# Performance work log

Hardware: AMD Instinct MI355X
Metric: run time of the kernel (lower is better)

Reference implementation:

```python
import jax, jax.numpy as jnp
import numpy as np

DIM = 512
DEPTH = 6
HEADS = 8
DH = 64
WS = 256
INNER = HEADS * DH  # 512
FF_INNER = int(DIM * 4 * 2 / 3)  # 1365
QK_SCALE = 8.0


def l2norm(x):
    n = jnp.linalg.norm(x, axis=-1, keepdims=True)
    return x / jnp.maximum(n, 1e-12)


def rotate_half(x):
    x1, x2 = jnp.split(x, 2, axis=-1)
    return jnp.concatenate([-x2, x1], axis=-1)


def apply_xpos_rotary(q, k, n, dh, scale_base):
    # SinusoidalEmbeddings with use_xpos=True, scale_base = window_size // 2
    inv_freq = 1.0 / (10000.0 ** (jnp.arange(0, dh, 2, dtype=jnp.float32) / dh))  # (dh/2,)
    t = jnp.arange(n, dtype=jnp.float32)
    freqs = t[:, None] * inv_freq[None, :]                     # (n, dh/2)
    freqs = jnp.concatenate([freqs, freqs], axis=-1)           # (n, dh)
    sv = (jnp.arange(0, dh, 2, dtype=jnp.float32) + 0.4 * dh) / (1.4 * dh)  # (dh/2,)
    power = (t - n // 2) / scale_base
    xs = sv[None, :] ** power[:, None]                         # (n, dh/2)
    xs = jnp.concatenate([xs, xs], axis=-1)                    # (n, dh)
    cos, sin = jnp.cos(freqs), jnp.sin(freqs)
    q = q * cos * xs + rotate_half(q) * sin * xs
    k = k * cos / xs + rotate_half(k) * sin / xs
    return q, k


def local_mha(x, Wqkv, Wo, q_scale, k_scale):
    b, n, d = x.shape
    qkv = x @ Wqkv                                             # (b, n, 3*INNER)
    q, k, v = jnp.split(qkv, 3, axis=-1)
    to_heads = lambda t: t.reshape(b, n, HEADS, DH).transpose(0, 2, 1, 3)
    q, k, v = to_heads(q), to_heads(k), to_heads(v)            # (b, h, n, dh)
    # qk rmsnorm (l2 norm + learned per-dim scale), fixed attn scale = 8
    q = l2norm(q) * q_scale
    k = l2norm(k) * k_scale
    q, k = apply_xpos_rotary(q, k, n, DH, WS // 2)
    w = n // WS
    bucket = lambda t: t.reshape(b, HEADS, w, WS, DH)
    bq, bk, bv = bucket(q), bucket(k), bucket(v)
    # look_around: prepend previous window (look_backward=1, look_forward=0)
    def look_around(t):
        prev = jnp.concatenate([jnp.zeros_like(t[:, :, :1]), t[:, :, :-1]], axis=2)
        return jnp.concatenate([prev, t], axis=3)              # (b, h, w, 2*WS, dh)
    bk2, bv2 = look_around(bk), look_around(bv)
    # positions and masks (causal + exact windowsize + pad)
    tq = jnp.arange(n, dtype=jnp.int32).reshape(w, WS)
    tk_prev = jnp.concatenate([jnp.full((1, WS), -1, dtype=jnp.int32), tq[:-1]], axis=0)
    tk = jnp.concatenate([tk_prev, tq], axis=1)                # (w, 2*WS)
    diff = tq[:, :, None] - tk[:, None, :]
    allowed = (diff >= 0) & (diff <= WS) & (tk[:, None, :] >= 0)  # (w, WS, 2*WS)
    sim = jnp.einsum('bhwie,bhwje->bhwij', bq, bk2) * QK_SCALE
    sim = jnp.where(allowed, sim, -jnp.finfo(sim.dtype).max)
    attn = jax.nn.softmax(sim, axis=-1)
    o = jnp.einsum('bhwij,bhwje->bhwie', attn, bv2)            # (b, h, w, WS, dh)
    o = o.reshape(b, HEADS, n, DH).transpose(0, 2, 1, 3).reshape(b, n, INNER)
    return o @ Wo


def feedforward(x, W1, b1, W2, b2):
    h = x @ W1 + b1
    a, g = jnp.split(h, 2, axis=-1)
    return (a * jax.nn.gelu(g, approximate=False)) @ W2 + b2


def setup_inputs() -> dict:
    key = jax.random.key(0)
    ks = jax.random.split(key, 8)
    s = 0.02
    x = jax.random.normal(ks[0], (1, 8192, DIM), dtype=jnp.float32)
    Wqkv = jax.random.normal(ks[1], (DEPTH, DIM, 3 * INNER), dtype=jnp.float32) * s
    Wo = jax.random.normal(ks[2], (DEPTH, INNER, DIM), dtype=jnp.float32) * s
    q_scale = jnp.ones((DEPTH, DH), dtype=jnp.float32)
    k_scale = jnp.ones((DEPTH, DH), dtype=jnp.float32)
    W1 = jax.random.normal(ks[3], (DEPTH, DIM, 2 * FF_INNER), dtype=jnp.float32) * s
    b1 = jnp.zeros((DEPTH, 2 * FF_INNER), dtype=jnp.float32)
    W2 = jax.random.normal(ks[4], (DEPTH, FF_INNER, DIM), dtype=jnp.float32) * s
    b2 = jnp.zeros((DEPTH, DIM), dtype=jnp.float32)
    return {"x": x, "Wqkv": Wqkv, "Wo": Wo, "q_scale": q_scale, "k_scale": k_scale,
            "W1": W1, "b1": b1, "W2": W2, "b2": b2}


def reference(x, Wqkv, Wo, q_scale, k_scale, W1, b1, W2, b2):
    for i in range(DEPTH):
        x = local_mha(x, Wqkv[i], Wo[i], q_scale[i], k_scale[i]) + x
        x = feedforward(x, W1[i], b1[i], W2[i], b2[i]) + x
    return x
```

## Files before the change

### kernel.cpp

```cpp
#include <hip/hip_runtime.h>
#include <hip/hip_bf16.h>
#include <math.h>

typedef short s16x8 __attribute__((ext_vector_type(8)));
typedef short s16x4 __attribute__((ext_vector_type(4)));
typedef float f32x4 __attribute__((ext_vector_type(4)));

#define MFMA(A,B,C) __builtin_amdgcn_mfma_f32_16x16x32_bf16((A),(B),(C),0,0,0)

typedef __attribute__((address_space(3))) unsigned int lds_u32;
typedef __attribute__((address_space(1))) const unsigned int glb_u32;
__device__ __forceinline__ void gload16(const short* g, const short* l){
  __builtin_amdgcn_global_load_lds((glb_u32*)g, (lds_u32*)l, 16, 0, 0);
}

__device__ __forceinline__ float bf2f(short u){
  unsigned int x = ((unsigned int)(unsigned short)u) << 16;
  return __builtin_bit_cast(float, x);
}
__device__ __forceinline__ short f2bf(float f){
  unsigned int x = __builtin_bit_cast(unsigned int, f);
  x += 0x7fffu + ((x >> 16) & 1u);
  return (short)(x >> 16);
}
__device__ __forceinline__ float gelu_t(float x){
  float u = x + 0.044715f*x*x*x;
  float e = __expf(1.5957691216057308f*u);
  float th = 1.f - 2.f/(e + 1.f);
  return 0.5f*x*(1.f + th);
}

__device__ __forceinline__ void xcd_swz(int gx, int gy, int &bx, int &by){
  int id = bx + by*gx;
  int nwg = gx*gy;
  int q = nwg >> 3, r = nwg & 7;
  int xcd = id & 7, idx = id >> 3;
  int nid = (xcd < r ? xcd*(q+1) : r*(q+1) + (xcd-r)*q) + idx;
  bx = nid % gx; by = nid / gx;
}

#define FFI 1365
#define FFIP 1376

template<int HAS_BIAS, int HAS_RES, int OUT_F32, int OUT_BF16>
__global__ __launch_bounds__(512) void gemm_k(
    const short* __restrict__ A, const short* __restrict__ Bt,
    const float* __restrict__ bias, const float* __restrict__ res,
    float* __restrict__ outF, short* __restrict__ outB,
    int M, int N, int K)
{
  __shared__ short As[2][128*32];
  __shared__ short Bs[2][128*32];
  const int tid = threadIdx.x;
  const int lane = tid & 63, wv = tid >> 6;
  const int g = lane >> 4, qi = lane & 15;
  int bx = blockIdx.x, by = blockIdx.y;
  xcd_swz(gridDim.x, gridDim.y, bx, by);
  const int m0 = bx * 128, n0 = by * 128;
  const int wm = (wv >> 2) * 64, wn = (wv & 3) * 32;

  const int sr = tid >> 2, sc = (tid & 3) * 8;
  const short* Ag = A  + (size_t)(m0 + sr)*K + sc;
  const short* Bg = Bt + (size_t)(n0 + sr)*K + sc;

  f32x4 acc[4][2];
  #pragma unroll
  for (int i=0;i<4;i++)
    #pragma unroll
    for (int j=0;j<2;j++) acc[i][j] = (f32x4){0.f,0.f,0.f,0.f};

  auto stage = [&](int buf, int k0){
    gload16(Ag + k0, &As[buf][wv*512]);
    gload16(Bg + k0, &Bs[buf][wv*512]);
  };

  const int nt = K >> 5;
  stage(0, 0);
  __syncthreads();
  for (int t = 0; t < nt; ++t) {
    const int cur = t & 1;
    if (t + 1 < nt) stage(cur ^ 1, (t+1) << 5);
    s16x8 af[4], bf[2];
    #pragma unroll
    for (int mi=0;mi<4;mi++) af[mi] = *(const s16x8*)&As[cur][(wm+mi*16+qi)*32 + g*8];
    #pragma unroll
    for (int ni=0;ni<2;ni++) bf[ni] = *(const s16x8*)&Bs[cur][(wn+ni*16+qi)*32 + g*8];
    #pragma unroll
    for (int mi=0;mi<4;mi++)
      #pragma unroll
      for (int ni=0;ni<2;ni++)
        acc[mi][ni] = MFMA(af[mi], bf[ni], acc[mi][ni]);
    __syncthreads();
  }
  #pragma unroll
  for (int mi=0;mi<4;mi++){
    #pragma unroll
    for (int r=0;r<4;r++){
      int row = m0 + wm + mi*16 + g*4 + r;
      #pragma unroll
      for (int ni=0;ni<2;ni++){
        int col = n0 + wn + ni*16 + qi;
        float v = acc[mi][ni][r];
        if (HAS_BIAS) v += bias[col];
        if (HAS_RES)  v += res[(size_t)row*N + col];
        if (OUT_F32)  outF[(size_t)row*N + col] = v;
        if (OUT_BF16) outB[(size_t)row*N + col] = f2bf(v);
      }
    }
  }
}

__global__ __launch_bounds__(512) void geglu_k(
    const short* __restrict__ A, const short* __restrict__ Bt,
    const float* __restrict__ b1, short* __restrict__ hg)
{
  __shared__ short As[2][128*32];
  __shared__ short Ba[2][128*32];
  __shared__ short Bg[2][128*32];
  const int tid = threadIdx.x;
  const int lane = tid & 63, wv = tid >> 6;
  const int g = lane >> 4, qi = lane & 15;
  int bx = blockIdx.x, by = blockIdx.y;
  xcd_swz(gridDim.x, gridDim.y, bx, by);
  const int m0 = bx * 128, n0 = by * 128;
  const int wm = (wv >> 2) * 64, wn = (wv & 3) * 32;

  const int sr = tid >> 2, sc = (tid & 3) * 8;
  const short* Ag = A + (size_t)(m0 + sr)*512 + sc;
  const short* Pa = Bt + (size_t)min(n0 + sr, FFI-1)*512 + sc;
  const short* Pg = Bt + (size_t)min(FFI + n0 + sr, 2729)*512 + sc;

  f32x4 aa[4][2], ag[4][2];
  #pragma unroll
  for (int i=0;i<4;i++)
    #pragma unroll
    for (int j=0;j<2;j++){ aa[i][j]=(f32x4){0.f,0.f,0.f,0.f}; ag[i][j]=(f32x4){0.f,0.f,0.f,0.f}; }

  auto stage = [&](int buf, int k0){
    gload16(Ag + k0, &As[buf][wv*512]);
    gload16(Pa + k0, &Ba[buf][wv*512]);
    gload16(Pg + k0, &Bg[buf][wv*512]);
  };

  stage(0, 0);
  __syncthreads();
  for (int t = 0; t < 16; ++t) {
    const int cur = t & 1;
    if (t + 1 < 16) stage(cur ^ 1, (t+1) << 5);
    s16x8 af[4], bfa[2], bfg[2];
    #pragma unroll
    for (int mi=0;mi<4;mi++) af[mi] = *(const s16x8*)&As[cur][(wm+mi*16+qi)*32 + g*8];
    #pragma unroll
    for (int ni=0;ni<2;ni++){ bfa[ni] = *(const s16x8*)&Ba[cur][(wn+ni*16+qi)*32 + g*8];
                              bfg[ni] = *(const s16x8*)&Bg[cur][(wn+ni*16+qi)*32 + g*8]; }
    #pragma unroll
    for (int mi=0;mi<4;mi++)
      #pragma unroll
      for (int ni=0;ni<2;ni++){
        aa[mi][ni] = MFMA(af[mi], bfa[ni], aa[mi][ni]);
        ag[mi][ni] = MFMA(af[mi], bfg[ni], ag[mi][ni]);
      }
    __syncthreads();
  }
  #pragma unroll
  for (int mi=0;mi<4;mi++){
    #pragma unroll
    for (int r=0;r<4;r++){
      int row = m0 + wm + mi*16 + g*4 + r;
      #pragma unroll
      for (int ni=0;ni<2;ni++){
        int col = n0 + wn + ni*16 + qi;
        if (col < FFI){
          float va = aa[mi][ni][r] + b1[col];
          float vg = ag[mi][ni][r] + b1[FFI+col];
          hg[(size_t)row*FFIP + col] = f2bf(va * gelu_t(vg));
        } else if (col < FFIP){
          hg[(size_t)row*FFIP + col] = 0;
        }
      }
    }
  }
}

__global__ void rope_k(float* __restrict__ tab){
  int n = blockIdx.x, dd = threadIdx.x;
  int i = dd & 31;
  double invf = pow(10000.0, -(double)i/32.0);
  double fr = (double)n * invf;
  double c = cos(fr), s = sin(fr);
  double sv = (2.0*i + 25.6)/89.6;
  double pw = ((double)n - 4096.0)/128.0;
  double xs = pow(sv, pw);
  size_t o = (size_t)n*64 + dd;
  tab[o]            = (float)(c*xs);
  tab[524288+o]     = (float)(s*xs);
  tab[2*524288+o]   = (float)(c/xs);
  tab[3*524288+o]   = (float)(s/xs);
}

__global__ __launch_bounds__(256) void wtrans_k(
    const float* __restrict__ src, short* __restrict__ dst,
    int K, int N, int Kp, long srcStride, long dstStride)
{
  __shared__ float t[64][65];
  const float* s = src + (size_t)blockIdx.z * srcStride;
  short* d = dst + (size_t)blockIdx.z * dstStride;
  int n0 = blockIdx.x*64, k0 = blockIdx.y*64;
  int tid = threadIdx.x;
  #pragma unroll
  for (int p=0;p<4;p++){
    int task = p*256+tid;
    int r = task>>4, c = (task&15)*4;
    int k = k0 + r;
    #pragma unroll
    for (int e=0;e<4;e++){
      int n = n0+c+e;
      t[r][c+e] = (k<K && n<N) ? s[(size_t)k*N+n] : 0.f;
    }
  }
  __syncthreads();
  #pragma unroll
  for (int p=0;p<2;p++){
    int task = p*256+tid;
    int nr = task>>3, kg=(task&7)*8;
    int n = n0+nr;
    if (n < N && (k0+kg) < Kp){
      s16x8 v;
      #pragma unroll
      for (int j=0;j<8;j++) v[j] = f2bf(t[kg+j][nr]);
      *(s16x8*)(d + (size_t)n*Kp + k0 + kg) = v;
    }
  }
}

__global__ void cast_k(const float* __restrict__ in, short* __restrict__ out){
  int i = (blockIdx.x*256+threadIdx.x)*4;
  float4 v = *(const float4*)(in+i);
  s16x4 o = { f2bf(v.x), f2bf(v.y), f2bf(v.z), f2bf(v.w) };
  *(s16x4*)(out+i) = o;
}

__global__ __launch_bounds__(256) void qkprep_k(
    const short* __restrict__ qkv, const float* __restrict__ tab,
    const float* __restrict__ qs, const float* __restrict__ ks,
    short* __restrict__ qrot, short* __restrict__ krot)
{
  int wv = threadIdx.x >> 6, lane = threadIdx.x & 63;
  int wid = blockIdx.x*4 + wv;
  int n = wid >> 3, h = wid & 7;
  float qv = bf2f(qkv[(size_t)n*1536 + h*64 + lane]);
  float kv = bf2f(qkv[(size_t)n*1536 + 512 + h*64 + lane]);
  float sq = qv*qv, sk = kv*kv;
  #pragma unroll
  for (int m=1;m<64;m<<=1){ sq += __shfl_xor(sq,m,64); sk += __shfl_xor(sk,m,64); }
  qv *= qs[lane] / fmaxf(sqrtf(sq), 1e-12f);
  kv *= ks[lane] / fmaxf(sqrtf(sk), 1e-12f);
  float qo = __shfl_xor(qv,32,64), ko = __shfl_xor(kv,32,64);
  float sgn = (lane<32)? -1.f : 1.f;
  size_t to = (size_t)n*64 + lane;
  float cq = tab[to], sxq = tab[524288+to], ck = tab[2*524288+to], sxk = tab[3*524288+to];
  qrot[((size_t)h*8192+n)*64+lane] = f2bf(qv*cq + sgn*qo*sxq);
  krot[((size_t)h*8192+n)*64+lane] = f2bf(kv*ck + sgn*ko*sxk);
}

__global__ __launch_bounds__(256) void vtrans_k(const short* __restrict__ qkv, short* __restrict__ vt){
  __shared__ short t[64][72];
  int n0 = blockIdx.x*64, h = blockIdx.y;
  int tid = threadIdx.x;
  #pragma unroll
  for (int p=0;p<2;p++){
    int task = p*256+tid;
    int r = task>>3, cg = (task&7)*8;
    *(s16x8*)&t[r][cg] = *(const s16x8*)(qkv + (size_t)(n0+r)*1536 + 1024 + h*64 + cg);
  }
  __syncthreads();
  #pragma unroll
  for (int p=0;p<2;p++){
    int task = p*256+tid;
    int d = task>>3, nb = (task&7)*8;
    s16x8 v;
    #pragma unroll
    for (int j=0;j<8;j++) v[j] = t[nb+j][d];
    *(s16x8*)(vt + ((size_t)h*64+d)*8192 + n0 + nb) = v;
  }
}

__global__ __launch_bounds__(512,1) void attn_k(
    const short* __restrict__ qrot, const short* __restrict__ krot,
    const short* __restrict__ vt, short* __restrict__ attn_o)
{
  __shared__ short Ks[128][72];
  __shared__ short Vs[64][136];
  const int w = blockIdx.x, h = blockIdx.y;
  const int tid = threadIdx.x, lane = tid & 63, wv = tid >> 6;
  const int g = lane >> 4, qi = lane & 15;
  const int wq0 = wv * 32;
  s16x8 qf[2][2];
  #pragma unroll
  for (int ni=0;ni<2;ni++){
    int qg = w*256 + wq0 + ni*16 + qi;
    const short* p = qrot + ((size_t)h*8192 + qg)*64 + g*8;
    qf[ni][0] = *(const s16x8*)p;
    qf[ni][1] = *(const s16x8*)(p + 32);
  }
  f32x4 oacc[4][2];
  float mrun[2], lrun[2];
  #pragma unroll
  for (int i=0;i<2;i++){
    mrun[i] = -1e30f; lrun[i] = 0.f;
    #pragma unroll
    for (int j=0;j<4;j++) oacc[j][i]=(f32x4){0.f,0.f,0.f,0.f};
  }
  const int kvbase = w*256 - 256;
  for (int s=0;s<4;s++){
    __syncthreads();
    #pragma unroll
    for (int p=0;p<2;p++){
      int task = p*512 + tid;
      {
        int r = task>>3, cg = (task&7)*8;
        int jg = kvbase + s*128 + r;
        s16x8 v = {0,0,0,0,0,0,0,0};
        if (jg>=0) v = *(const s16x8*)(krot + ((size_t)h*8192+jg)*64 + cg);
        *(s16x8*)&Ks[r][cg] = v;
      }
      {
        int dd = task>>4, cg = (task&15)*8;
        int jg = kvbase + s*128 + cg;
        s16x8 v = {0,0,0,0,0,0,0,0};
        if (jg>=0) v = *(const s16x8*)(vt + ((size_t)h*64+dd)*8192 + jg);
        *(s16x8*)&Vs[dd][cg] = v;
      }
    }
    __syncthreads();
    for (int cc=0;cc<2;cc++){
      const int jlo = (s*2+cc)*64;
      if (jlo + 63 < wq0) continue;
      if (jlo > wq0 + 287) continue;
      if (w==0 && jlo < 256) continue;
      f32x4 sacc[4][2];
      #pragma unroll
      for (int i=0;i<4;i++)
        #pragma unroll
        for (int j=0;j<2;j++) sacc[i][j]=(f32x4){0.f,0.f,0.f,0.f};
      #pragma unroll
      for (int ks=0;ks<2;ks++){
        s16x8 kf[4];
        #pragma unroll
        for (int mi=0;mi<4;mi++) kf[mi] = *(const s16x8*)&Ks[cc*64+mi*16+qi][ks*32+g*8];
        #pragma unroll
        for (int mi=0;mi<4;mi++)
          #pragma unroll
          for (int ni=0;ni<2;ni++)
            sacc[mi][ni] = MFMA(kf[mi], qf[ni][ks], sacc[mi][ni]);
      }
      const bool interior = (jlo >= wq0+31) && (jlo+63 <= wq0+256);
      float cmax[2];
      #pragma unroll
      for (int ni=0;ni<2;ni++) cmax[ni] = -1e30f;
      #pragma unroll
      for (int mi=0;mi<4;mi++)
        #pragma unroll
        for (int ni=0;ni<2;ni++)
          #pragma unroll
          for (int r=0;r<4;r++){
            float x = sacc[mi][ni][r] * 8.f;
            if (!interior){
              int j = jlo + mi*16 + g*4 + r;
              int ql = wq0 + ni*16 + qi;
              if (j < ql || j > ql+256) x = -1e30f;
            }
            sacc[mi][ni][r] = x;
            cmax[ni] = fmaxf(cmax[ni], x);
          }
      #pragma unroll
      for (int ni=0;ni<2;ni++){
        cmax[ni] = fmaxf(cmax[ni], __shfl_xor(cmax[ni],16,64));
        cmax[ni] = fmaxf(cmax[ni], __shfl_xor(cmax[ni],32,64));
      }
      float scl[2], psum[2];
      s16x8 pf[2][2];
      #pragma unroll
      for (int ni=0;ni<2;ni++){
        float mn = fmaxf(mrun[ni], cmax[ni]);
        scl[ni] = __expf(mrun[ni]-mn);
        mrun[ni] = mn;
        float ps = 0.f;
        #pragma unroll
        for (int t=0;t<2;t++)
          #pragma unroll
          for (int hh=0; hh<2; hh++){
            int mi = 2*t+hh;
            #pragma unroll
            for (int r=0;r<4;r++){
              float pv = __expf(sacc[mi][ni][r]-mn);
              ps += pv;
              pf[t][ni][hh*4+r] = f2bf(pv);
            }
          }
        psum[ni]=ps;
      }
      #pragma unroll
      for (int ni=0;ni<2;ni++){
        psum[ni] += __shfl_xor(psum[ni],16,64);
        psum[ni] += __shfl_xor(psum[ni],32,64);
        lrun[ni] = lrun[ni]*scl[ni] + psum[ni];
        #pragma unroll
        for (int mi=0;mi<4;mi++) oacc[mi][ni] *= scl[ni];
      }
      #pragma unroll
      for (int t=0;t<2;t++)
        #pragma unroll
        for (int mi=0;mi<4;mi++){
          const short* vp = &Vs[mi*16+qi][cc*64 + t*32 + g*4];
          s16x4 lo = *(const s16x4*)vp;
          s16x4 hi = *(const s16x4*)(vp+16);
          s16x8 vf = {lo[0],lo[1],lo[2],lo[3],hi[0],hi[1],hi[2],hi[3]};
          #pragma unroll
          for (int ni=0;ni<2;ni++)
            oacc[mi][ni] = MFMA(vf, pf[t][ni], oacc[mi][ni]);
        }
    }
  }
  #pragma unroll
  for (int ni=0;ni<2;ni++){
    float inv = 1.f / lrun[ni];
    int qg = w*256 + wq0 + ni*16 + qi;
    #pragma unroll
    for (int mi=0;mi<4;mi++){
      s16x4 st;
      #pragma unroll
      for (int r=0;r<4;r++) st[r] = f2bf(oacc[mi][ni][r]*inv);
      *(s16x4*)(attn_o + (size_t)qg*512 + h*64 + mi*16 + g*4) = st;
    }
  }
}

extern "C" void kernel_launch(void* const* d_in, const int* in_sizes, int n_in,
                              void* d_out, int out_size, void* d_ws, size_t ws_size,
                              hipStream_t stream)
{
  const float* x_in = (const float*)d_in[0];
  const float* Wqkv = (const float*)d_in[1];
  const float* Wo   = (const float*)d_in[2];
  const float* qsc  = (const float*)d_in[3];
  const float* ksc  = (const float*)d_in[4];
  const float* W1   = (const float*)d_in[5];
  const float* b1   = (const float*)d_in[6];
  const float* W2   = (const float*)d_in[7];
  const float* b2   = (const float*)d_in[8];
  float* xf = (float*)d_out;

  char* ws = (char*)d_ws;
  size_t off = 0;
  float* tab  = (float*)(ws + off); off += (size_t)4*8192*64*4;
  short* WqkvT= (short*)(ws + off); off += (size_t)6*1536*512*2;
  short* WoT  = (short*)(ws + off); off += (size_t)6*512*512*2;
  short* W1T  = (short*)(ws + off); off += (size_t)6*2730*512*2;
  short* W2T  = (short*)(ws + off); off += (size_t)6*512*1376*2;
  short* xbf  = (short*)(ws + off); off += (size_t)8192*512*2;
  short* qkv  = (short*)(ws + off); off += (size_t)8192*1536*2;
  short* qrot = (short*)(ws + off); off += (size_t)8*8192*64*2;
  short* krot = (short*)(ws + off); off += (size_t)8*8192*64*2;
  short* vt   = (short*)(ws + off); off += (size_t)8*8192*64*2;
  short* attno= (short*)(ws + off); off += (size_t)8192*512*2;
  short* hg   = (short*)(ws + off); off += (size_t)8192*1376*2;

  hipMemcpyAsync(xf, x_in, (size_t)8192*512*4, hipMemcpyDeviceToDevice, stream);
  rope_k<<<8192, 64, 0, stream>>>(tab);
  wtrans_k<<<dim3(24,8,6),256,0,stream>>>(Wqkv, WqkvT, 512,1536,512, (long)512*1536, (long)1536*512);
  wtrans_k<<<dim3(8,8,6),256,0,stream>>>(Wo, WoT, 512,512,512, (long)512*512,(long)512*512);
  wtrans_k<<<dim3(43,8,6),256,0,stream>>>(W1, W1T, 512,2730,512, (long)512*2730,(long)2730*512);
  wtrans_k<<<dim3(8,22,6),256,0,stream>>>(W2, W2T, 1365,512,1376, (long)1365*512,(long)512*1376);
  cast_k<<<4096,256,0,stream>>>(x_in, xbf);

  for (int l=0;l<6;l++){
    gemm_k<0,0,0,1><<<dim3(64,12),512,0,stream>>>(xbf, WqkvT + (size_t)l*1536*512,
        nullptr, nullptr, nullptr, qkv, 8192,1536,512);
    qkprep_k<<<16384,256,0,stream>>>(qkv, tab, qsc + l*64, ksc + l*64, qrot, krot);
    vtrans_k<<<dim3(128,8),256,0,stream>>>(qkv, vt);
    attn_k<<<dim3(32,8),512,0,stream>>>(qrot, krot, vt, attno);
    gemm_k<0,1,1,1><<<dim3(64,4),512,0,stream>>>(attno, WoT + (size_t)l*512*512,
        nullptr, xf, xf, xbf, 8192,512,512);
    geglu_k<<<dim3(64,11),512,0,stream>>>(xbf, W1T + (size_t)l*2730*512, b1 + (size_t)l*2730, hg);
    gemm_k<1,1,1,1><<<dim3(64,4),512,0,stream>>>(hg, W2T + (size_t)l*512*1376,
        b2 + (size_t)l*512, xf, xf, xbf, 8192,512,1376);
  }
}
```

Before: 1.200 ms.

## Triple-buffer LDS staging in GEMM and GeGLU kernels with one barrier per step

Moves the GEMM and GeGLU kernels from double to triple LDS buffering. Loads are issued two K-steps ahead, and an explicit vmcnt wait replaces the full __syncthreads. This leaves one barrier per iteration instead of one after the load wait and another after compute, aiming to hide more global-load latency and cut sync stalls. The cost is more LDS per block (72KB for geglu), which may lower occupancy. It also relies on careful vmcnt counting, since the barrier is what stops a buffer being overwritten while it is still being read.

```diff
diff --git a/kernel.cpp b/kernel.cpp
--- a/kernel.cpp
+++ b/kernel.cpp
@@ -7,6 +7,8 @@
 typedef float f32x4 __attribute__((ext_vector_type(4)));
 
 #define MFMA(A,B,C) __builtin_amdgcn_mfma_f32_16x16x32_bf16((A),(B),(C),0,0,0)
+#define WAITV(N) asm volatile("s_waitcnt vmcnt(" #N ")" ::: "memory")
+#define FENCE()  asm volatile("" ::: "memory")
 
 typedef __attribute__((address_space(3))) unsigned int lds_u32;
 typedef __attribute__((address_space(1))) const unsigned int glb_u32;
@@ -49,8 +51,8 @@
     float* __restrict__ outF, short* __restrict__ outB,
     int M, int N, int K)
 {
-  __shared__ short As[2][128*32];
-  __shared__ short Bs[2][128*32];
+  __shared__ short As[3][128*32];
+  __shared__ short Bs[3][128*32];
   const int tid = threadIdx.x;
   const int lane = tid & 63, wv = tid >> 6;
   const int g = lane >> 4, qi = lane & 15;
@@ -69,28 +71,32 @@
     #pragma unroll
     for (int j=0;j<2;j++) acc[i][j] = (f32x4){0.f,0.f,0.f,0.f};
 
-  auto stage = [&](int buf, int k0){
+  auto stage = [&](int buf, int t){
+    int k0 = t << 5;
     gload16(Ag + k0, &As[buf][wv*512]);
     gload16(Bg + k0, &Bs[buf][wv*512]);
   };
 
   const int nt = K >> 5;
   stage(0, 0);
-  __syncthreads();
+  stage(1, 1);
+  int cb = 0, sb = 2;
   for (int t = 0; t < nt; ++t) {
-    const int cur = t & 1;
-    if (t + 1 < nt) stage(cur ^ 1, (t+1) << 5);
+    if (t + 1 < nt) { WAITV(2); } else { WAITV(0); }
+    __builtin_amdgcn_s_barrier();
+    FENCE();
+    if (t + 2 < nt) { stage(sb, t+2); sb = (sb==2)?0:sb+1; }
     s16x8 af[4], bf[2];
     #pragma unroll
-    for (int mi=0;mi<4;mi++) af[mi] = *(const s16x8*)&As[cur][(wm+mi*16+qi)*32 + g*8];
-    #pragma unroll
-    for (int ni=0;ni<2;ni++) bf[ni] = *(const s16x8*)&Bs[cur][(wn+ni*16+qi)*32 + g*8];
+    for (int mi=0;mi<4;mi++) af[mi] = *(const s16x8*)&As[cb][(wm+mi*16+qi)*32 + g*8];
+    #pragma unroll
+    for (int ni=0;ni<2;ni++) bf[ni] = *(const s16x8*)&Bs[cb][(wn+ni*16+qi)*32 + g*8];
     #pragma unroll
     for (int mi=0;mi<4;mi++)
       #pragma unroll
       for (int ni=0;ni<2;ni++)
         acc[mi][ni] = MFMA(af[mi], bf[ni], acc[mi][ni]);
-    __syncthreads();
+    cb = (cb==2)?0:cb+1;
   }
   #pragma unroll
   for (int mi=0;mi<4;mi++){
@@ -114,9 +120,9 @@
     const short* __restrict__ A, const short* __restrict__ Bt,
     const float* __restrict__ b1, short* __restrict__ hg)
 {
-  __shared__ short As[2][128*32];
-  __shared__ short Ba[2][128*32];
-  __shared__ short Bg[2][128*32];
+  __shared__ short As[3][128*32];
+  __shared__ short Ba[3][128*32];
+  __shared__ short Bg[3][128*32];
   const int tid = threadIdx.x;
   const int lane = tid & 63, wv = tid >> 6;
   const int g = lane >> 4, qi = lane & 15;
@@ -136,23 +142,27 @@
     #pragma unroll
     for (int j=0;j<2;j++){ aa[i][j]=(f32x4){0.f,0.f,0.f,0.f}; ag[i][j]=(f32x4){0.f,0.f,0.f,0.f}; }
 
-  auto stage = [&](int buf, int k0){
+  auto stage = [&](int buf, int t){
+    int k0 = t << 5;
     gload16(Ag + k0, &As[buf][wv*512]);
     gload16(Pa + k0, &Ba[buf][wv*512]);
     gload16(Pg + k0, &Bg[buf][wv*512]);
   };
 
   stage(0, 0);
-  __syncthreads();
+  stage(1, 1);
+  int cb = 0, sb = 2;
   for (int t = 0; t < 16; ++t) {
-    const int cur = t & 1;
-    if (t + 1 < 16) stage(cur ^ 1, (t+1) << 5);
+    if (t + 1 < 16) { WAITV(3); } else { WAITV(0); }
+    __builtin_amdgcn_s_barrier();
+    FENCE();
+    if (t + 2 < 16) { stage(sb, t+2); sb = (sb==2)?0:sb+1; }
     s16x8 af[4], bfa[2], bfg[2];
     #pragma unroll
-    for (int mi=0;mi<4;mi++) af[mi] = *(const s16x8*)&As[cur][(wm+mi*16+qi)*32 + g*8];
-    #pragma unroll
-    for (int ni=0;ni<2;ni++){ bfa[ni] = *(const s16x8*)&Ba[cur][(wn+ni*16+qi)*32 + g*8];
-                              bfg[ni] = *(const s16x8*)&Bg[cur][(wn+ni*16+qi)*32 + g*8]; }
+    for (int mi=0;mi<4;mi++) af[mi] = *(const s16x8*)&As[cb][(wm+mi*16+qi)*32 + g*8];
+    #pragma unroll
+    for (int ni=0;ni<2;ni++){ bfa[ni] = *(const s16x8*)&Ba[cb][(wn+ni*16+qi)*32 + g*8];
+                              bfg[ni] = *(const s16x8*)&Bg[cb][(wn+ni*16+qi)*32 + g*8]; }
     #pragma unroll
     for (int mi=0;mi<4;mi++)
       #pragma unroll
@@ -160,7 +170,7 @@
         aa[mi][ni] = MFMA(af[mi], bfa[ni], aa[mi][ni]);
         ag[mi][ni] = MFMA(af[mi], bfg[ni], ag[mi][ni]);
       }
-    __syncthreads();
+    cb = (cb==2)?0:cb+1;
   }
   #pragma unroll
   for (int mi=0;mi<4;mi++){
```

Result: slower. 1.227 ms (+2.2%).

## Restructure GEMMs to stream A from registers and stage full-K swizzled B in LDS

Applied to the files above, without the earlier changes.

Replaces the double-buffered 128x128 LDS-staged GEMM and GEGLU kernels with 256-thread kernels. Each wave loads its A fragments directly from global memory into registers with software prefetch, and a large K-chunk of B (64 columns) is staged once into XOR-swizzled LDS, so there are far fewer barriers per K loop. The W2 transpose is padded to a K stride of 1536 so the FF-out GEMM can run in three 512-wide chunks; the hg buffer gets slack space for the over-read past column 1376. The aim is to cut LDS traffic and synchronisation, at the cost of more register pressure and uncoalesced direct global loads of A.

```diff
diff --git a/kernel.cpp b/kernel.cpp
--- a/kernel.cpp
+++ b/kernel.cpp
@@ -7,12 +7,6 @@
 typedef float f32x4 __attribute__((ext_vector_type(4)));
 
 #define MFMA(A,B,C) __builtin_amdgcn_mfma_f32_16x16x32_bf16((A),(B),(C),0,0,0)
-
-typedef __attribute__((address_space(3))) unsigned int lds_u32;
-typedef __attribute__((address_space(1))) const unsigned int glb_u32;
-__device__ __forceinline__ void gload16(const short* g, const short* l){
-  __builtin_amdgcn_global_load_lds((glb_u32*)g, (lds_u32*)l, 16, 0, 0);
-}
 
 __device__ __forceinline__ float bf2f(short u){
   unsigned int x = ((unsigned int)(unsigned short)u) << 16;
@@ -42,65 +36,77 @@
 #define FFI 1365
 #define FFIP 1376
 
-template<int HAS_BIAS, int HAS_RES, int OUT_F32, int OUT_BF16>
-__global__ __launch_bounds__(512) void gemm_k(
+template<int MF, int KSTEPS, int NKC, int HAS_BIAS, int HAS_RES, int OUT_F32, int OUT_BF16>
+__global__ __launch_bounds__(256) void gemm_s(
     const short* __restrict__ A, const short* __restrict__ Bt,
     const float* __restrict__ bias, const float* __restrict__ res,
     float* __restrict__ outF, short* __restrict__ outB,
-    int M, int N, int K)
+    int N, int KstA, int KstB)
 {
-  __shared__ short As[2][128*32];
-  __shared__ short Bs[2][128*32];
+  constexpr int K4 = KSTEPS*4;
+  constexpr int BKC = KSTEPS*32;
+  __shared__ short Bs[64*K4*8];
   const int tid = threadIdx.x;
   const int lane = tid & 63, wv = tid >> 6;
   const int g = lane >> 4, qi = lane & 15;
   int bx = blockIdx.x, by = blockIdx.y;
   xcd_swz(gridDim.x, gridDim.y, bx, by);
-  const int m0 = bx * 128, n0 = by * 128;
-  const int wm = (wv >> 2) * 64, wn = (wv & 3) * 32;
-
-  const int sr = tid >> 2, sc = (tid & 3) * 8;
-  const short* Ag = A  + (size_t)(m0 + sr)*K + sc;
-  const short* Bg = Bt + (size_t)(n0 + sr)*K + sc;
-
-  f32x4 acc[4][2];
-  #pragma unroll
-  for (int i=0;i<4;i++)
-    #pragma unroll
-    for (int j=0;j<2;j++) acc[i][j] = (f32x4){0.f,0.f,0.f,0.f};
-
-  auto stage = [&](int buf, int k0){
-    gload16(Ag + k0, &As[buf][wv*512]);
-    gload16(Bg + k0, &Bs[buf][wv*512]);
-  };
-
-  const int nt = K >> 5;
-  stage(0, 0);
-  __syncthreads();
-  for (int t = 0; t < nt; ++t) {
-    const int cur = t & 1;
-    if (t + 1 < nt) stage(cur ^ 1, (t+1) << 5);
-    s16x8 af[4], bf[2];
-    #pragma unroll
-    for (int mi=0;mi<4;mi++) af[mi] = *(const s16x8*)&As[cur][(wm+mi*16+qi)*32 + g*8];
-    #pragma unroll
-    for (int ni=0;ni<2;ni++) bf[ni] = *(const s16x8*)&Bs[cur][(wn+ni*16+qi)*32 + g*8];
-    #pragma unroll
-    for (int mi=0;mi<4;mi++)
-      #pragma unroll
-      for (int ni=0;ni<2;ni++)
-        acc[mi][ni] = MFMA(af[mi], bf[ni], acc[mi][ni]);
+  const int m0 = bx * (MF*64), n0 = by * 64;
+
+  const short* Ap = A + (size_t)(m0 + wv*(MF*16) + qi)*KstA + g*8;
+
+  f32x4 acc[MF][4];
+  #pragma unroll
+  for (int i=0;i<MF;i++)
+    #pragma unroll
+    for (int j=0;j<4;j++) acc[i][j] = (f32x4){0.f,0.f,0.f,0.f};
+
+  s16x8 a0[MF], a1[MF], a2[MF], a3[MF];
+
+  for (int kc=0; kc<NKC; ++kc){
+    if (kc) __syncthreads();
+    #pragma unroll
+    for (int p=0; p<KSTEPS; ++p){
+      int slot = p*256 + tid;
+      int r = slot / K4;
+      int s = slot & (K4-1);
+      s16x8 v = *(const s16x8*)(Bt + (size_t)(n0+r)*KstB + kc*BKC + s*8);
+      *(s16x8*)&Bs[((r*K4) + (s^(r&7)))*8] = v;
+    }
+    const short* Apc = Ap + kc*BKC;
+    auto LOADA = [&](s16x8 (&buf)[MF], int kk){
+      #pragma unroll
+      for (int mf=0; mf<MF; ++mf)
+        buf[mf] = *(const s16x8*)(Apc + (size_t)mf*16*KstA + kk*32);
+    };
+    LOADA(a0,0); LOADA(a1,1); LOADA(a2,2); LOADA(a3,3);
     __syncthreads();
-  }
-  #pragma unroll
-  for (int mi=0;mi<4;mi++){
-    #pragma unroll
-    for (int r=0;r<4;r++){
-      int row = m0 + wm + mi*16 + g*4 + r;
-      #pragma unroll
-      for (int ni=0;ni<2;ni++){
-        int col = n0 + wn + ni*16 + qi;
-        float v = acc[mi][ni][r];
+    auto STEP = [&](s16x8 (&buf)[MF], int kk){
+      s16x8 bf[4];
+      #pragma unroll
+      for (int nf=0; nf<4; ++nf)
+        bf[nf] = *(const s16x8*)&Bs[(((nf*16+qi)*K4) + ((kk*4+g)^(qi&7)))*8];
+      #pragma unroll
+      for (int mf=0; mf<MF; ++mf)
+        #pragma unroll
+        for (int nf=0; nf<4; ++nf)
+          acc[mf][nf] = MFMA(buf[mf], bf[nf], acc[mf][nf]);
+      if (kk+4 < KSTEPS) LOADA(buf, kk+4);
+    };
+    #pragma unroll
+    for (int kk=0; kk<KSTEPS; kk+=4){
+      STEP(a0,kk); STEP(a1,kk+1); STEP(a2,kk+2); STEP(a3,kk+3);
+    }
+  }
+  #pragma unroll
+  for (int mf=0; mf<MF; ++mf){
+    #pragma unroll
+    for (int rr=0; rr<4; ++rr){
+      int row = m0 + wv*(MF*16) + mf*16 + g*4 + rr;
+      #pragma unroll
+      for (int nf=0; nf<4; ++nf){
+        int col = n0 + nf*16 + qi;
+        float v = acc[mf][nf][rr];
         if (HAS_BIAS) v += bias[col];
         if (HAS_RES)  v += res[(size_t)row*N + col];
         if (OUT_F32)  outF[(size_t)row*N + col] = v;
@@ -110,69 +116,86 @@
   }
 }
 
-__global__ __launch_bounds__(512) void geglu_k(
+__global__ __launch_bounds__(256) void geglu_s(
     const short* __restrict__ A, const short* __restrict__ Bt,
     const float* __restrict__ b1, short* __restrict__ hg)
 {
-  __shared__ short As[2][128*32];
-  __shared__ short Ba[2][128*32];
-  __shared__ short Bg[2][128*32];
+  constexpr int KSTEPS = 8, K4 = 32, BKC = 256;
+  __shared__ short Ba[64*K4*8];
+  __shared__ short Bg[64*K4*8];
   const int tid = threadIdx.x;
   const int lane = tid & 63, wv = tid >> 6;
   const int g = lane >> 4, qi = lane & 15;
   int bx = blockIdx.x, by = blockIdx.y;
   xcd_swz(gridDim.x, gridDim.y, bx, by);
-  const int m0 = bx * 128, n0 = by * 128;
-  const int wm = (wv >> 2) * 64, wn = (wv & 3) * 32;
-
-  const int sr = tid >> 2, sc = (tid & 3) * 8;
-  const short* Ag = A + (size_t)(m0 + sr)*512 + sc;
-  const short* Pa = Bt + (size_t)min(n0 + sr, FFI-1)*512 + sc;
-  const short* Pg = Bt + (size_t)min(FFI + n0 + sr, 2729)*512 + sc;
-
-  f32x4 aa[4][2], ag[4][2];
+  const int m0 = bx * 256, n0 = by * 64;
+
+  const short* Ap = A + (size_t)(m0 + wv*64 + qi)*512 + g*8;
+
+  f32x4 aa[4][4], ag[4][4];
   #pragma unroll
   for (int i=0;i<4;i++)
     #pragma unroll
-    for (int j=0;j<2;j++){ aa[i][j]=(f32x4){0.f,0.f,0.f,0.f}; ag[i][j]=(f32x4){0.f,0.f,0.f,0.f}; }
-
-  auto stage = [&](int buf, int k0){
-    gload16(Ag + k0, &As[buf][wv*512]);
-    gload16(Pa + k0, &Ba[buf][wv*512]);
-    gload16(Pg + k0, &Bg[buf][wv*512]);
-  };
-
-  stage(0, 0);
-  __syncthreads();
-  for (int t = 0; t < 16; ++t) {
-    const int cur = t & 1;
-    if (t + 1 < 16) stage(cur ^ 1, (t+1) << 5);
-    s16x8 af[4], bfa[2], bfg[2];
-    #pragma unroll
-    for (int mi=0;mi<4;mi++) af[mi] = *(const s16x8*)&As[cur][(wm+mi*16+qi)*32 + g*8];
-    #pragma unroll
-    for (int ni=0;ni<2;ni++){ bfa[ni] = *(const s16x8*)&Ba[cur][(wn+ni*16+qi)*32 + g*8];
-                              bfg[ni] = *(const s16x8*)&Bg[cur][(wn+ni*16+qi)*32 + g*8]; }
-    #pragma unroll
-    for (int mi=0;mi<4;mi++)
-      #pragma unroll
-      for (int ni=0;ni<2;ni++){
-        aa[mi][ni] = MFMA(af[mi], bfa[ni], aa[mi][ni]);
-        ag[mi][ni] = MFMA(af[mi], bfg[ni], ag[mi][ni]);
-      }
+    for (int j=0;j<4;j++){ aa[i][j]=(f32x4){0.f,0.f,0.f,0.f}; ag[i][j]=(f32x4){0.f,0.f,0.f,0.f}; }
+
+  s16x8 a0[4], a1[4];
+
+  for (int kc=0; kc<2; ++kc){
+    if (kc) __syncthreads();
+    #pragma unroll
+    for (int p=0; p<KSTEPS; ++p){
+      int slot = p*256 + tid;
+      int r = slot / K4;
+      int s = slot & (K4-1);
+      int ra = min(n0 + r, FFI-1);
+      int rg = min(FFI + n0 + r, 2729);
+      s16x8 va = *(const s16x8*)(Bt + (size_t)ra*512 + kc*BKC + s*8);
+      s16x8 vg = *(const s16x8*)(Bt + (size_t)rg*512 + kc*BKC + s*8);
+      int sw = ((r*K4) + (s^(r&7)))*8;
+      *(s16x8*)&Ba[sw] = va;
+      *(s16x8*)&Bg[sw] = vg;
+    }
+    const short* Apc = Ap + kc*BKC;
+    auto LOADA = [&](s16x8 (&buf)[4], int kk){
+      #pragma unroll
+      for (int mf=0; mf<4; ++mf)
+        buf[mf] = *(const s16x8*)(Apc + (size_t)mf*16*512 + kk*32);
+    };
+    LOADA(a0,0); LOADA(a1,1);
     __syncthreads();
-  }
-  #pragma unroll
-  for (int mi=0;mi<4;mi++){
-    #pragma unroll
-    for (int r=0;r<4;r++){
-      int row = m0 + wm + mi*16 + g*4 + r;
-      #pragma unroll
-      for (int ni=0;ni<2;ni++){
-        int col = n0 + wn + ni*16 + qi;
+    auto STEP = [&](s16x8 (&buf)[4], int kk){
+      s16x8 ba[4], bg[4];
+      #pragma unroll
+      for (int nf=0; nf<4; ++nf){
+        int off = (((nf*16+qi)*K4) + ((kk*4+g)^(qi&7)))*8;
+        ba[nf] = *(const s16x8*)&Ba[off];
+        bg[nf] = *(const s16x8*)&Bg[off];
+      }
+      #pragma unroll
+      for (int mf=0; mf<4; ++mf)
+        #pragma unroll
+        for (int nf=0; nf<4; ++nf){
+          aa[mf][nf] = MFMA(buf[mf], ba[nf], aa[mf][nf]);
+          ag[mf][nf] = MFMA(buf[mf], bg[nf], ag[mf][nf]);
+        }
+      if (kk+2 < KSTEPS) LOADA(buf, kk+2);
+    };
+    #pragma unroll
+    for (int kk=0; kk<KSTEPS; kk+=2){
+      STEP(a0,kk); STEP(a1,kk+1);
+    }
+  }
+  #pragma unroll
+  for (int mf=0; mf<4; ++mf){
+    #pragma unroll
+    for (int rr=0; rr<4; ++rr){
+      int row = m0 + wv*64 + mf*16 + g*4 + rr;
+      #pragma unroll
+      for (int nf=0; nf<4; ++nf){
+        int col = n0 + nf*16 + qi;
         if (col < FFI){
-          float va = aa[mi][ni][r] + b1[col];
-          float vg = ag[mi][ni][r] + b1[FFI+col];
+          float va = aa[mf][nf][rr] + b1[col];
+          float vg = ag[mf][nf][rr] + b1[FFI+col];
           hg[(size_t)row*FFIP + col] = f2bf(va * gelu_t(vg));
         } else if (col < FFIP){
           hg[(size_t)row*FFIP + col] = 0;
@@ -457,33 +480,33 @@
   short* WqkvT= (short*)(ws + off); off += (size_t)6*1536*512*2;
   short* WoT  = (short*)(ws + off); off += (size_t)6*512*512*2;
   short* W1T  = (short*)(ws + off); off += (size_t)6*2730*512*2;
-  short* W2T  = (short*)(ws + off); off += (size_t)6*512*1376*2;
+  short* W2T  = (short*)(ws + off); off += (size_t)6*512*1536*2;
   short* xbf  = (short*)(ws + off); off += (size_t)8192*512*2;
   short* qkv  = (short*)(ws + off); off += (size_t)8192*1536*2;
   short* qrot = (short*)(ws + off); off += (size_t)8*8192*64*2;
   short* krot = (short*)(ws + off); off += (size_t)8*8192*64*2;
   short* vt   = (short*)(ws + off); off += (size_t)8*8192*64*2;
   short* attno= (short*)(ws + off); off += (size_t)8192*512*2;
-  short* hg   = (short*)(ws + off); off += (size_t)8192*1376*2;
+  short* hg   = (short*)(ws + off); off += (size_t)8192*1376*2 + 4096;
 
   hipMemcpyAsync(xf, x_in, (size_t)8192*512*4, hipMemcpyDeviceToDevice, stream);
   rope_k<<<8192, 64, 0, stream>>>(tab);
   wtrans_k<<<dim3(24,8,6),256,0,stream>>>(Wqkv, WqkvT, 512,1536,512, (long)512*1536, (long)1536*512);
   wtrans_k<<<dim3(8,8,6),256,0,stream>>>(Wo, WoT, 512,512,512, (long)512*512,(long)512*512);
   wtrans_k<<<dim3(43,8,6),256,0,stream>>>(W1, W1T, 512,2730,512, (long)512*2730,(long)2730*512);
-  wtrans_k<<<dim3(8,22,6),256,0,stream>>>(W2, W2T, 1365,512,1376, (long)1365*512,(long)512*1376);
+  wtrans_k<<<dim3(8,24,6),256,0,stream>>>(W2, W2T, 1365,512,1536, (long)1365*512,(long)512*1536);
   cast_k<<<4096,256,0,stream>>>(x_in, xbf);
 
   for (int l=0;l<6;l++){
-    gemm_k<0,0,0,1><<<dim3(64,12),512,0,stream>>>(xbf, WqkvT + (size_t)l*1536*512,
-        nullptr, nullptr, nullptr, qkv, 8192,1536,512);
+    gemm_s<4,16,1, 0,0,0,1><<<dim3(32,24),256,0,stream>>>(xbf, WqkvT + (size_t)l*1536*512,
+        nullptr, nullptr, nullptr, qkv, 1536, 512, 512);
     qkprep_k<<<16384,256,0,stream>>>(qkv, tab, qsc + l*64, ksc + l*64, qrot, krot);
     vtrans_k<<<dim3(128,8),256,0,stream>>>(qkv, vt);
     attn_k<<<dim3(32,8),512,0,stream>>>(qrot, krot, vt, attno);
-    gemm_k<0,1,1,1><<<dim3(64,4),512,0,stream>>>(attno, WoT + (size_t)l*512*512,
-        nullptr, xf, xf, xbf, 8192,512,512);
-    geglu_k<<<dim3(64,11),512,0,stream>>>(xbf, W1T + (size_t)l*2730*512, b1 + (size_t)l*2730, hg);
-    gemm_k<1,1,1,1><<<dim3(64,4),512,0,stream>>>(hg, W2T + (size_t)l*512*1376,
-        b2 + (size_t)l*512, xf, xf, xbf, 8192,512,1376);
-  }
-}
+    gemm_s<2,16,1, 0,1,1,1><<<dim3(64,8),256,0,stream>>>(attno, WoT + (size_t)l*512*512,
+        nullptr, xf, xf, xbf, 512, 512, 512);
+    geglu_s<<<dim3(32,22),256,0,stream>>>(xbf, W1T + (size_t)l*2730*512, b1 + (size_t)l*2730, hg);
+    gemm_s<2,16,3, 1,1,1,1><<<dim3(64,8),256,0,stream>>>(hg, W2T + (size_t)l*512*1536,
+        b2 + (size_t)l*512, xf, xf, xbf, 512, 1376, 1536);
+  }
+}
```

Result: slower. 1.726 ms (+43.8%).

## Split attention blocks by query half, add 64x64 GEMM, batch qkprep rows

Applied to the files above, without the earlier changes.

The attention kernel now launches twice as many blocks. Each block covers half of a 256-query window, with one 16-query tile per wave, and loads only the three KV stages it needs. The N=512 output GEMMs (Wo and W2) move to a new 64x64-tile, 256-thread kernel with a 128x8 grid, which raises block count and occupancy on the many-CU device. qkprep processes 8 rows per wave and hoists the scale loads, cutting grid size. In exchange, K/V tiles are loaded redundantly across the two halves, and the smaller GEMM tiles get less operand reuse.

```diff
diff --git a/kernel.cpp b/kernel.cpp
--- a/kernel.cpp
+++ b/kernel.cpp
@@ -94,6 +94,74 @@
   }
   #pragma unroll
   for (int mi=0;mi<4;mi++){
+    #pragma unroll
+    for (int r=0;r<4;r++){
+      int row = m0 + wm + mi*16 + g*4 + r;
+      #pragma unroll
+      for (int ni=0;ni<2;ni++){
+        int col = n0 + wn + ni*16 + qi;
+        float v = acc[mi][ni][r];
+        if (HAS_BIAS) v += bias[col];
+        if (HAS_RES)  v += res[(size_t)row*N + col];
+        if (OUT_F32)  outF[(size_t)row*N + col] = v;
+        if (OUT_BF16) outB[(size_t)row*N + col] = f2bf(v);
+      }
+    }
+  }
+}
+
+template<int HAS_BIAS, int HAS_RES, int OUT_F32, int OUT_BF16>
+__global__ __launch_bounds__(256) void gemm64_k(
+    const short* __restrict__ A, const short* __restrict__ Bt,
+    const float* __restrict__ bias, const float* __restrict__ res,
+    float* __restrict__ outF, short* __restrict__ outB,
+    int M, int N, int K)
+{
+  __shared__ short As[2][64*32];
+  __shared__ short Bs[2][64*32];
+  const int tid = threadIdx.x;
+  const int lane = tid & 63, wv = tid >> 6;
+  const int g = lane >> 4, qi = lane & 15;
+  int bx = blockIdx.x, by = blockIdx.y;
+  xcd_swz(gridDim.x, gridDim.y, bx, by);
+  const int m0 = bx * 64, n0 = by * 64;
+  const int wm = (wv >> 1) * 32, wn = (wv & 1) * 32;
+
+  const int sr = tid >> 2, sc = (tid & 3) * 8;
+  const short* Ag = A  + (size_t)(m0 + sr)*K + sc;
+  const short* Bg = Bt + (size_t)(n0 + sr)*K + sc;
+
+  f32x4 acc[2][2];
+  #pragma unroll
+  for (int i=0;i<2;i++)
+    #pragma unroll
+    for (int j=0;j<2;j++) acc[i][j] = (f32x4){0.f,0.f,0.f,0.f};
+
+  auto stage = [&](int buf, int k0){
+    gload16(Ag + k0, &As[buf][wv*512]);
+    gload16(Bg + k0, &Bs[buf][wv*512]);
+  };
+
+  const int nt = K >> 5;
+  stage(0, 0);
+  __syncthreads();
+  for (int t = 0; t < nt; ++t) {
+    const int cur = t & 1;
+    if (t + 1 < nt) stage(cur ^ 1, (t+1) << 5);
+    s16x8 af[2], bf[2];
+    #pragma unroll
+    for (int mi=0;mi<2;mi++) af[mi] = *(const s16x8*)&As[cur][(wm+mi*16+qi)*32 + g*8];
+    #pragma unroll
+    for (int ni=0;ni<2;ni++) bf[ni] = *(const s16x8*)&Bs[cur][(wn+ni*16+qi)*32 + g*8];
+    #pragma unroll
+    for (int mi=0;mi<2;mi++)
+      #pragma unroll
+      for (int ni=0;ni<2;ni++)
+        acc[mi][ni] = MFMA(af[mi], bf[ni], acc[mi][ni]);
+    __syncthreads();
+  }
+  #pragma unroll
+  for (int mi=0;mi<2;mi++){
     #pragma unroll
     for (int r=0;r<4;r++){
       int row = m0 + wm + mi*16 + g*4 + r;
@@ -246,21 +314,25 @@
     short* __restrict__ qrot, short* __restrict__ krot)
 {
   int wv = threadIdx.x >> 6, lane = threadIdx.x & 63;
-  int wid = blockIdx.x*4 + wv;
-  int n = wid >> 3, h = wid & 7;
-  float qv = bf2f(qkv[(size_t)n*1536 + h*64 + lane]);
-  float kv = bf2f(qkv[(size_t)n*1536 + 512 + h*64 + lane]);
-  float sq = qv*qv, sk = kv*kv;
-  #pragma unroll
-  for (int m=1;m<64;m<<=1){ sq += __shfl_xor(sq,m,64); sk += __shfl_xor(sk,m,64); }
-  qv *= qs[lane] / fmaxf(sqrtf(sq), 1e-12f);
-  kv *= ks[lane] / fmaxf(sqrtf(sk), 1e-12f);
-  float qo = __shfl_xor(qv,32,64), ko = __shfl_xor(kv,32,64);
-  float sgn = (lane<32)? -1.f : 1.f;
-  size_t to = (size_t)n*64 + lane;
-  float cq = tab[to], sxq = tab[524288+to], ck = tab[2*524288+to], sxk = tab[3*524288+to];
-  qrot[((size_t)h*8192+n)*64+lane] = f2bf(qv*cq + sgn*qo*sxq);
-  krot[((size_t)h*8192+n)*64+lane] = f2bf(kv*ck + sgn*ko*sxk);
+  float qsc = qs[lane], ksc = ks[lane];
+  #pragma unroll
+  for (int it=0; it<8; ++it){
+    int wid = it*8192 + blockIdx.x*4 + wv;
+    int n = wid >> 3, h = wid & 7;
+    float qv = bf2f(qkv[(size_t)n*1536 + h*64 + lane]);
+    float kv = bf2f(qkv[(size_t)n*1536 + 512 + h*64 + lane]);
+    float sq = qv*qv, sk = kv*kv;
+    #pragma unroll
+    for (int m=1;m<64;m<<=1){ sq += __shfl_xor(sq,m,64); sk += __shfl_xor(sk,m,64); }
+    qv *= qsc / fmaxf(sqrtf(sq), 1e-12f);
+    kv *= ksc / fmaxf(sqrtf(sk), 1e-12f);
+    float qo = __shfl_xor(qv,32,64), ko = __shfl_xor(kv,32,64);
+    float sgn = (lane<32)? -1.f : 1.f;
+    size_t to = (size_t)n*64 + lane;
+    float cq = tab[to], sxq = tab[524288+to], ck = tab[2*524288+to], sxk = tab[3*524288+to];
+    qrot[((size_t)h*8192+n)*64+lane] = f2bf(qv*cq + sgn*qo*sxq);
+    krot[((size_t)h*8192+n)*64+lane] = f2bf(kv*ck + sgn*ko*sxk);
+  }
 }
 
 __global__ __launch_bounds__(256) void vtrans_k(const short* __restrict__ qkv, short* __restrict__ vt){
@@ -291,28 +363,24 @@
 {
   __shared__ short Ks[128][72];
   __shared__ short Vs[64][136];
-  const int w = blockIdx.x, h = blockIdx.y;
+  const int bxx = blockIdx.x, h = blockIdx.y;
+  const int w = bxx >> 1, half = bxx & 1;
   const int tid = threadIdx.x, lane = tid & 63, wv = tid >> 6;
   const int g = lane >> 4, qi = lane & 15;
-  const int wq0 = wv * 32;
-  s16x8 qf[2][2];
-  #pragma unroll
-  for (int ni=0;ni<2;ni++){
-    int qg = w*256 + wq0 + ni*16 + qi;
-    const short* p = qrot + ((size_t)h*8192 + qg)*64 + g*8;
-    qf[ni][0] = *(const s16x8*)p;
-    qf[ni][1] = *(const s16x8*)(p + 32);
-  }
-  f32x4 oacc[4][2];
-  float mrun[2], lrun[2];
-  #pragma unroll
-  for (int i=0;i<2;i++){
-    mrun[i] = -1e30f; lrun[i] = 0.f;
-    #pragma unroll
-    for (int j=0;j<4;j++) oacc[j][i]=(f32x4){0.f,0.f,0.f,0.f};
-  }
+  const int wq = half*128 + wv*16;
+  const int q0abs = w*256 + wq;
+  s16x8 qf[2];
+  {
+    const short* p = qrot + ((size_t)h*8192 + q0abs + qi)*64 + g*8;
+    qf[0] = *(const s16x8*)p;
+    qf[1] = *(const s16x8*)(p + 32);
+  }
+  f32x4 oacc[4];
+  #pragma unroll
+  for (int j=0;j<4;j++) oacc[j]=(f32x4){0.f,0.f,0.f,0.f};
+  float mrun = -1e30f, lrun = 0.f;
   const int kvbase = w*256 - 256;
-  for (int s=0;s<4;s++){
+  for (int s=half; s<half+3; ++s){
     __syncthreads();
     #pragma unroll
     for (int p=0;p<2;p++){
@@ -334,15 +402,13 @@
     }
     __syncthreads();
     for (int cc=0;cc<2;cc++){
-      const int jlo = (s*2+cc)*64;
-      if (jlo + 63 < wq0) continue;
-      if (jlo > wq0 + 287) continue;
+      const int jlo = s*128 + cc*64;
+      if (jlo + 63 < wq) continue;
+      if (jlo > wq + 271) continue;
       if (w==0 && jlo < 256) continue;
-      f32x4 sacc[4][2];
-      #pragma unroll
-      for (int i=0;i<4;i++)
-        #pragma unroll
-        for (int j=0;j<2;j++) sacc[i][j]=(f32x4){0.f,0.f,0.f,0.f};
+      f32x4 sacc[4];
+      #pragma unroll
+      for (int i=0;i<4;i++) sacc[i]=(f32x4){0.f,0.f,0.f,0.f};
       #pragma unroll
       for (int ks=0;ks<2;ks++){
         s16x8 kf[4];
@@ -350,64 +416,47 @@
         for (int mi=0;mi<4;mi++) kf[mi] = *(const s16x8*)&Ks[cc*64+mi*16+qi][ks*32+g*8];
         #pragma unroll
         for (int mi=0;mi<4;mi++)
-          #pragma unroll
-          for (int ni=0;ni<2;ni++)
-            sacc[mi][ni] = MFMA(kf[mi], qf[ni][ks], sacc[mi][ni]);
-      }
-      const bool interior = (jlo >= wq0+31) && (jlo+63 <= wq0+256);
-      float cmax[2];
-      #pragma unroll
-      for (int ni=0;ni<2;ni++) cmax[ni] = -1e30f;
+          sacc[mi] = MFMA(kf[mi], qf[ks], sacc[mi]);
+      }
+      const bool interior = (jlo >= wq+15) && (jlo+63 <= wq+256);
+      float cmax = -1e30f;
       #pragma unroll
       for (int mi=0;mi<4;mi++)
         #pragma unroll
-        for (int ni=0;ni<2;ni++)
+        for (int r=0;r<4;r++){
+          float x = sacc[mi][r] * 8.f;
+          if (!interior){
+            int j = jlo + mi*16 + g*4 + r;
+            int ql = wq + qi;
+            if (j < ql || j > ql+256) x = -1e30f;
+          }
+          sacc[mi][r] = x;
+          cmax = fmaxf(cmax, x);
+        }
+      cmax = fmaxf(cmax, __shfl_xor(cmax,16,64));
+      cmax = fmaxf(cmax, __shfl_xor(cmax,32,64));
+      float mn = fmaxf(mrun, cmax);
+      float scl = __expf(mrun - mn);
+      mrun = mn;
+      float ps = 0.f;
+      s16x8 pf[2];
+      #pragma unroll
+      for (int t=0;t<2;t++)
+        #pragma unroll
+        for (int hh=0; hh<2; hh++){
+          int mi = 2*t+hh;
           #pragma unroll
           for (int r=0;r<4;r++){
-            float x = sacc[mi][ni][r] * 8.f;
-            if (!interior){
-              int j = jlo + mi*16 + g*4 + r;
-              int ql = wq0 + ni*16 + qi;
-              if (j < ql || j > ql+256) x = -1e30f;
-            }
-            sacc[mi][ni][r] = x;
-            cmax[ni] = fmaxf(cmax[ni], x);
+            float pv = __expf(sacc[mi][r]-mn);
+            ps += pv;
+            pf[t][hh*4+r] = f2bf(pv);
           }
-      #pragma unroll
-      for (int ni=0;ni<2;ni++){
-        cmax[ni] = fmaxf(cmax[ni], __shfl_xor(cmax[ni],16,64));
-        cmax[ni] = fmaxf(cmax[ni], __shfl_xor(cmax[ni],32,64));
-      }
-      float scl[2], psum[2];
-      s16x8 pf[2][2];
-      #pragma unroll
-      for (int ni=0;ni<2;ni++){
-        float mn = fmaxf(mrun[ni], cmax[ni]);
-        scl[ni] = __expf(mrun[ni]-mn);
-        mrun[ni] = mn;
-        float ps = 0.f;
-        #pragma unroll
-        for (int t=0;t<2;t++)
-          #pragma unroll
-          for (int hh=0; hh<2; hh++){
-            int mi = 2*t+hh;
-            #pragma unroll
-            for (int r=0;r<4;r++){
-              float pv = __expf(sacc[mi][ni][r]-mn);
-              ps += pv;
-              pf[t][ni][hh*4+r] = f2bf(pv);
-            }
-          }
-        psum[ni]=ps;
-      }
-      #pragma unroll
-      for (int ni=0;ni<2;ni++){
-        psum[ni] += __shfl_xor(psum[ni],16,64);
-        psum[ni] += __shfl_xor(psum[ni],32,64);
-        lrun[ni] = lrun[ni]*scl[ni] + psum[ni];
-        #pragma unroll
-        for (int mi=0;mi<4;mi++) oacc[mi][ni] *= scl[ni];
-      }
+        }
+      ps += __shfl_xor(ps,16,64);
+      ps += __shfl_xor(ps,32,64);
+      lrun = lrun*scl + ps;
+      #pragma unroll
+      for (int mi=0;mi<4;mi++) oacc[mi] *= scl;
       #pragma unroll
       for (int t=0;t<2;t++)
         #pragma unroll
@@ -416,23 +465,17 @@
           s16x4 lo = *(const s16x4*)vp;
           s16x4 hi = *(const s16x4*)(vp+16);
           s16x8 vf = {lo[0],lo[1],lo[2],lo[3],hi[0],hi[1],hi[2],hi[3]};
-          #pragma unroll
-          for (int ni=0;ni<2;ni++)
-            oacc[mi][ni] = MFMA(vf, pf[t][ni], oacc[mi][ni]);
+          oacc[mi] = MFMA(vf, pf[t], oacc[mi]);
         }
     }
   }
-  #pragma unroll
-  for (int ni=0;ni<2;ni++){
-    float inv = 1.f / lrun[ni];
-    int qg = w*256 + wq0 + ni*16 + qi;
-    #pragma unroll
-    for (int mi=0;mi<4;mi++){
-      s16x4 st;
-      #pragma unroll
-      for (int r=0;r<4;r++) st[r] = f2bf(oacc[mi][ni][r]*inv);
-      *(s16x4*)(attn_o + (size_t)qg*512 + h*64 + mi*16 + g*4) = st;
-    }
+  float inv = 1.f / lrun;
+  #pragma unroll
+  for (int mi=0;mi<4;mi++){
+    s16x4 st;
+    #pragma unroll
+    for (int r=0;r<4;r++) st[r] = f2bf(oacc[mi][r]*inv);
+    *(s16x4*)(attn_o + (size_t)(q0abs+qi)*512 + h*64 + mi*16 + g*4) = st;
   }
 }
 
@@ -477,13 +520,13 @@
   for (int l=0;l<6;l++){
     gemm_k<0,0,0,1><<<dim3(64,12),512,0,stream>>>(xbf, WqkvT + (size_t)l*1536*512,
         nullptr, nullptr, nullptr, qkv, 8192,1536,512);
-    qkprep_k<<<16384,256,0,stream>>>(qkv, tab, qsc + l*64, ksc + l*64, qrot, krot);
+    qkprep_k<<<2048,256,0,stream>>>(qkv, tab, qsc + l*64, ksc + l*64, qrot, krot);
     vtrans_k<<<dim3(128,8),256,0,stream>>>(qkv, vt);
-    attn_k<<<dim3(32,8),512,0,stream>>>(qrot, krot, vt, attno);
-    gemm_k<0,1,1,1><<<dim3(64,4),512,0,stream>>>(attno, WoT + (size_t)l*512*512,
+    attn_k<<<dim3(64,8),512,0,stream>>>(qrot, krot, vt, attno);
+    gemm64_k<0,1,1,1><<<dim3(128,8),256,0,stream>>>(attno, WoT + (size_t)l*512*512,
         nullptr, xf, xf, xbf, 8192,512,512);
     geglu_k<<<dim3(64,11),512,0,stream>>>(xbf, W1T + (size_t)l*2730*512, b1 + (size_t)l*2730, hg);
-    gemm_k<1,1,1,1><<<dim3(64,4),512,0,stream>>>(hg, W2T + (size_t)l*512*1376,
+    gemm64_k<1,1,1,1><<<dim3(128,8),256,0,stream>>>(hg, W2T + (size_t)l*512*1376,
         b2 + (size_t)l*512, xf, xf, xbf, 8192,512,1376);
   }
 }
```

Result: faster. 1.146 ms (-4.6%).
